# Performance work log

Hardware: AMD Instinct MI355X
Metric: run time of the kernel (lower is better)

## Reference

```python
import jax, jax.numpy as jnp
import numpy as np

B, L_SEQ = 2, 2048
D, H, DF, NL, V = 1024, 16, 4096, 3, 32000
E = D // H
EPS = 1e-5


def _ln(x, g, b):
    m = jnp.mean(x, axis=-1, keepdims=True)
    v = jnp.mean((x - m) ** 2, axis=-1, keepdims=True)
    return (x - m) * jax.lax.rsqrt(v + EPS) * g + b


def setup_inputs() -> dict:
    key = jax.random.key(0)
    ks = jax.random.split(key, 16)
    s = 0.02
    tokens = jax.random.randint(ks[0], (B, L_SEQ), 0, V)
    pad_mask = jnp.zeros((B, L_SEQ, 1), dtype=bool)
    inp = dict(
        tokens=tokens,
        pad_mask=pad_mask,
        tok_emb=jax.random.normal(ks[1], (V, D)) * s,
        pos_emb=jax.random.normal(ks[2], (L_SEQ, D)) * s,
        Wq=jax.random.normal(ks[3], (NL, D, D)) * s,
        bq=jnp.zeros((NL, D)),
        Wk=jax.random.normal(ks[4], (NL, D, D)) * s,
        bk=jnp.zeros((NL, D)),
        Wv=jax.random.normal(ks[5], (NL, D, D)) * s,
        bv=jnp.zeros((NL, D)),
        Wo=jax.random.normal(ks[6], (NL, D, D)) * s,
        bo=jnp.zeros((NL, D)),
        W1=jax.random.normal(ks[7], (NL, D, DF)) * s,
        b1=jnp.zeros((NL, DF)),
        W2=jax.random.normal(ks[8], (NL, DF, D)) * s,
        b2=jnp.zeros((NL, D)),
        ln1_g=jnp.ones((NL, D)), ln1_b=jnp.zeros((NL, D)),
        ln3_g=jnp.ones((NL, D)), ln3_b=jnp.zeros((NL, D)),
        lnf_g=jnp.ones((D,)), lnf_b=jnp.zeros((D,)),
        Wout=jax.random.normal(ks[9], (D, V)) * s,
        bout=jnp.zeros((V,)),
    )
    return inp


def reference(tokens, pad_mask, tok_emb, pos_emb, Wq, bq, Wk, bk, Wv, bv,
              Wo, bo, W1, b1, W2, b2, ln1_g, ln1_b, ln3_g, ln3_b,
              lnf_g, lnf_b, Wout, bout):
    Bb, Ls = tokens.shape
    x = tok_emb[tokens] + pos_emb[:Ls]  # [B,L,D]
    causal = jnp.triu(jnp.ones((Ls, Ls), dtype=bool), 1)
    # pad mask applied on keys, causal on (query,key); mask True = blocked
    mask = jnp.logical_or(pad_mask[:, :, 0][:, None, :], causal[None])  # [B,L,L]
    mask = mask[:, None]  # [B,1,L,L], broadcast over heads
    scale = 1.0 / np.sqrt(E)
    for i in range(NL):
        h = _ln(x, ln1_g[i], ln1_b[i])
        q = (h @ Wq[i] + bq[i]).reshape(Bb, Ls, H, E)
        k = (h @ Wk[i] + bk[i]).reshape(Bb, Ls, H, E)
        v = (h @ Wv[i] + bv[i]).reshape(Bb, Ls, H, E)
        scores = jnp.einsum('blhe,bshe->bhls', q, k)
        scores = jnp.where(mask, -jnp.inf, scores)
        A = jax.nn.softmax(scale * scores, axis=-1)
        A = jnp.where(mask, 0.0, A)
        o = jnp.einsum('bhls,bshd->blhd', A, v).reshape(Bb, Ls, D)
        x = x + (o @ Wo[i] + bo[i])
        h = _ln(x, ln3_g[i], ln3_b[i])
        h = jax.nn.gelu(h @ W1[i] + b1[i], approximate=False)
        x = x + (h @ W2[i] + b2[i])
    x = _ln(x, lnf_g, lnf_b)
    return x @ Wout + bout  # [B,L,V]
```

## Files before the change

kernel.cpp:

```cpp
#include <hip/hip_runtime.h>
#include <math.h>

#define D_    1024
#define H_    16
#define E_    64
#define DF_   4096
#define NL_   3
#define V_    32000
#define B_    2
#define LSEQ_ 2048
#define M_    (B_*LSEQ_)
#define QKVW  (3*D_)

#define OQKV  0
#define OWO   ((size_t)3072*1024)
#define OW1   ((size_t)4096*1024)
#define OW2   ((size_t)8192*1024)

typedef __attribute__((ext_vector_type(8))) short bf16x8;
typedef __attribute__((ext_vector_type(4))) float f32x4;
typedef __attribute__((ext_vector_type(4))) unsigned short us4_t;

__device__ __forceinline__ float bfr2f(unsigned short u){ return __uint_as_float(((unsigned)u)<<16); }
__device__ __forceinline__ unsigned short f2bfr(float f){
  unsigned u = __float_as_uint(f);
  u += 0x7fffu + ((u>>16)&1u);
  return (unsigned short)(u>>16);
}
__device__ __forceinline__ void gl_lds16(const unsigned short* g, unsigned short* l){
  __builtin_amdgcn_global_load_lds((const __attribute__((address_space(1))) void*)g,
                                   (__attribute__((address_space(3))) void*)l, 16, 0, 0);
}

__device__ __forceinline__ void row_ln_write(float4 v, const float* __restrict__ g,
                                             const float* __restrict__ b,
                                             unsigned short* __restrict__ hrow,
                                             float* red, int tid){
  const int wave = tid>>6, lane = tid&63;
  float s  = v.x+v.y+v.z+v.w;
  float s2 = v.x*v.x+v.y*v.y+v.z*v.z+v.w*v.w;
  #pragma unroll
  for (int off=1; off<64; off<<=1){ s += __shfl_xor(s,off); s2 += __shfl_xor(s2,off); }
  if (!lane){ red[wave]=s; red[4+wave]=s2; }
  __syncthreads();
  s  = red[0]+red[1]+red[2]+red[3];
  s2 = red[4]+red[5]+red[6]+red[7];
  const float mean = s*(1.f/D_);
  const float var  = s2*(1.f/D_) - mean*mean;
  const float rstd = rsqrtf(var + 1e-5f);
  float4 gg = ((const float4*)g)[tid];
  float4 bb = ((const float4*)b)[tid];
  us4_t ov;
  ov[0] = f2bfr((v.x-mean)*rstd*gg.x + bb.x);
  ov[1] = f2bfr((v.y-mean)*rstd*gg.y + bb.y);
  ov[2] = f2bfr((v.z-mean)*rstd*gg.z + bb.z);
  ov[3] = f2bfr((v.w-mean)*rstd*gg.w + bb.w);
  *(us4_t*)&hrow[tid*4] = ov;
}

__global__ __launch_bounds__(256) void embed_ln_kernel(const int* __restrict__ tokens,
                                                       const float* __restrict__ tok_emb,
                                                       const float* __restrict__ pos_emb,
                                                       const float* __restrict__ g,
                                                       const float* __restrict__ b,
                                                       float* __restrict__ x,
                                                       unsigned short* __restrict__ h){
  __shared__ float red[8];
  const int r = blockIdx.x, tid = threadIdx.x;
  const int l = r & (LSEQ_-1);
  const int t = tokens[r];
  float4 te = ((const float4*)(tok_emb + (size_t)t*D_))[tid];
  float4 pe = ((const float4*)(pos_emb + (size_t)l*D_))[tid];
  float4 o = {te.x+pe.x, te.y+pe.y, te.z+pe.z, te.w+pe.w};
  ((float4*)(x + (size_t)r*D_))[tid] = o;
  row_ln_write(o, g, b, h + (size_t)r*D_, red, tid);
}

__global__ __launch_bounds__(256) void ln_kernel(const float* __restrict__ x,
                                                 const float* __restrict__ g,
                                                 const float* __restrict__ b,
                                                 unsigned short* __restrict__ h){
  __shared__ float red[8];
  const int r = blockIdx.x, tid = threadIdx.x;
  float4 v = ((const float4*)(x + (size_t)r*D_))[tid];
  row_ln_write(v, g, b, h + (size_t)r*D_, red, tid);
}

__global__ __launch_bounds__(256) void reduce2_ln_kernel(float* __restrict__ x,
                                                         const float* __restrict__ pt,
                                                         const float* __restrict__ bias,
                                                         const float* __restrict__ g,
                                                         const float* __restrict__ b,
                                                         unsigned short* __restrict__ h){
  __shared__ float red[8];
  const int r = blockIdx.x, tid = threadIdx.x;
  const size_t i = ((size_t)r*D_ + tid*4);
  float4 xv = *(const float4*)(x + i);
  float4 p0 = *(const float4*)(pt + i);
  float4 p1 = *(const float4*)(pt + (size_t)M_*D_ + i);
  float4 bb = *(const float4*)(bias + tid*4);
  xv.x += p0.x + p1.x + bb.x;
  xv.y += p0.y + p1.y + bb.y;
  xv.z += p0.z + p1.z + bb.z;
  xv.w += p0.w + p1.w + bb.w;
  *(float4*)(x + i) = xv;
  row_ln_write(xv, g, b, h + (size_t)r*D_, red, tid);
}

__global__ __launch_bounds__(256) void transpose_layer_kernel(const float* __restrict__ Wq,
                                                              const float* __restrict__ Wk,
                                                              const float* __restrict__ Wv,
                                                              const float* __restrict__ Wo,
                                                              const float* __restrict__ W1,
                                                              const float* __restrict__ W2,
                                                              unsigned short* __restrict__ wt){
  __shared__ unsigned short T[64*65];
  const int bid = blockIdx.x, tid = threadIdx.x;
  const float* W; unsigned short* dst; int N, K, n0, k0;
  if (bid < 768){
    int z = bid>>8, t = bid&255;
    W = (z==0)?Wq:(z==1)?Wk:Wv; N=1024; K=1024;
    n0=(t&15)*64; k0=(t>>4)*64;
    dst = wt + OQKV + (size_t)z*1024*1024;
  } else if (bid < 1024){
    int t = bid-768; W=Wo; N=1024; K=1024;
    n0=(t&15)*64; k0=(t>>4)*64; dst = wt + OWO;
  } else if (bid < 2048){
    int t = bid-1024; W=W1; N=4096; K=1024;
    n0=(t&63)*64; k0=(t>>6)*64; dst = wt + OW1;
  } else {
    int t = bid-2048; W=W2; N=1024; K=4096;
    n0=(t&15)*64; k0=(t>>4)*64; dst = wt + OW2;
  }
  const int rr = tid>>4, c4 = (tid&15)*4;
  #pragma unroll
  for (int pp=0; pp<4; pp++){
    int row = pp*16 + rr;
    float4 f = *(const float4*)(W + (size_t)(k0+row)*N + n0 + c4);
    T[(c4+0)*65 + row] = f2bfr(f.x);
    T[(c4+1)*65 + row] = f2bfr(f.y);
    T[(c4+2)*65 + row] = f2bfr(f.z);
    T[(c4+3)*65 + row] = f2bfr(f.w);
  }
  __syncthreads();
  const int nr = tid>>2, kc = (tid&3)*16;
  bf16x8 o0, o1;
  #pragma unroll
  for (int j=0;j<8;j++){ o0[j] = (short)T[nr*65 + kc + j];
                         o1[j] = (short)T[nr*65 + kc + 8 + j]; }
  *(bf16x8*)&dst[(size_t)(n0+nr)*K + k0 + kc]     = o0;
  *(bf16x8*)&dst[(size_t)(n0+nr)*K + k0 + kc + 8] = o1;
}

__global__ __launch_bounds__(256) void transpose_kernel(const float* __restrict__ W,
                                                        unsigned short* __restrict__ WT,
                                                        int N, int K, int rowOff){
  __shared__ unsigned short T[64*65];
  const int n0 = blockIdx.x*64, k0 = blockIdx.y*64;
  const int tid = threadIdx.x;
  const int rr = tid>>4, c4 = (tid&15)*4;
  #pragma unroll
  for (int pp=0; pp<4; pp++){
    int row = pp*16 + rr;
    float4 f = *(const float4*)(W + (size_t)(k0+row)*N + n0 + c4);
    T[(c4+0)*65 + row] = f2bfr(f.x);
    T[(c4+1)*65 + row] = f2bfr(f.y);
    T[(c4+2)*65 + row] = f2bfr(f.z);
    T[(c4+3)*65 + row] = f2bfr(f.w);
  }
  __syncthreads();
  const int nr = tid>>2, kc = (tid&3)*16;
  bf16x8 o0, o1;
  #pragma unroll
  for (int j=0;j<8;j++){ o0[j] = (short)T[nr*65 + kc + j];
                         o1[j] = (short)T[nr*65 + kc + 8 + j]; }
  *(bf16x8*)&WT[(size_t)(rowOff+n0+nr)*K + k0 + kc]     = o0;
  *(bf16x8*)&WT[(size_t)(rowOff+n0+nr)*K + k0 + kc + 8] = o1;
}

__global__ void concat_bias3(const float* __restrict__ bq,
                             const float* __restrict__ bk,
                             const float* __restrict__ bv,
                             float* __restrict__ d){
  int i = blockIdx.x*256 + threadIdx.x;
  int layer = i / QKVW, j = i % QKVW;
  d[i] = (j < D_) ? bq[layer*D_+j] : (j < 2*D_) ? bk[layer*D_+j-D_] : bv[layer*D_+j-2*D_];
}

template<int EPI>
__global__ __launch_bounds__(256) void gemm_bt(const unsigned short* __restrict__ A,
                                               const unsigned short* __restrict__ Bt,
                                               const float* __restrict__ bias,
                                               unsigned short* __restrict__ Cb,
                                               float* __restrict__ Cf,
                                               int K, int Klen, int ldc){
  __shared__ unsigned short As[128*64];
  __shared__ unsigned short Bs[128*64];
  const int tid = threadIdx.x;
  const int wave = tid>>6, lane = tid&63;
  const int m0 = blockIdx.x*128, n0 = blockIdx.y*128;
  const int kbase = blockIdx.z * Klen;
  const int wr = wave>>1, wc = wave&1;
  const unsigned short* Ab = A + (size_t)m0*K + kbase;
  const unsigned short* Bb = Bt + (size_t)n0*K + kbase;
  f32x4 acc[4][4] = {};
  int srow[4], sk[4];
  #pragma unroll
  for (int i=0;i<4;i++){
    int ci = i*256 + tid;
    srow[i] = ci>>3;
    sk[i]   = ((ci&7) ^ (srow[i]&7))*8;
  }
  for (int kt=0; kt<Klen; kt+=64){
    __syncthreads();
    #pragma unroll
    for (int i=0;i<4;i++){
      gl_lds16(Ab + (size_t)srow[i]*K + kt + sk[i], As + i*2048 + wave*512);
      gl_lds16(Bb + (size_t)srow[i]*K + kt + sk[i], Bs + i*2048 + wave*512);
    }
    __syncthreads();
    #pragma unroll
    for (int ks=0; ks<2; ks++){
      bf16x8 af[4], bfv[4];
      #pragma unroll
      for (int mi=0;mi<4;mi++){
        int row = wr*64 + mi*16 + (lane&15);
        int ch  = (ks*4 + (lane>>4)) ^ (row&7);
        af[mi] = *(const bf16x8*)&As[row*64 + ch*8];
      }
      #pragma unroll
      for (int ni=0;ni<4;ni++){
        int row = wc*64 + ni*16 + (lane&15);
        int ch  = (ks*4 + (lane>>4)) ^ (row&7);
        bfv[ni] = *(const bf16x8*)&Bs[row*64 + ch*8];
      }
      #pragma unroll
      for (int mi=0;mi<4;mi++)
        #pragma unroll
        for (int ni=0;ni<4;ni++)
          acc[mi][ni] = __builtin_amdgcn_mfma_f32_16x16x32_bf16(af[mi], bfv[ni], acc[mi][ni], 0,0,0);
    }
  }
  const int rq = (lane>>4)*4, cq = lane&15;
  float* Cfz = (EPI==5) ? (Cf + (size_t)blockIdx.z*M_*D_) : Cf;
  #pragma unroll
  for (int mi=0;mi<4;mi++){
    #pragma unroll
    for (int j=0;j<4;j++){
      int r = m0 + wr*64 + mi*16 + rq + j;
      #pragma unroll
      for (int ni=0;ni<4;ni++){
        int c = n0 + wc*64 + ni*16 + cq;
        if (EPI==2)      Cf[(size_t)r*D_ + c] += acc[mi][ni][j] + bias[c];
        else if (EPI==5) Cfz[(size_t)r*ldc + c] = acc[mi][ni][j];
        else             Cf[(size_t)r*ldc + c] = acc[mi][ni][j] + bias[c];
      }
    }
  }
}

#define GBAR()  do{ __builtin_amdgcn_s_barrier(); __builtin_amdgcn_sched_barrier(0); }while(0)
#define GPHASE(P, STAGE_STMT, TAIL_STMT) do{                                        \
    bf16x8 afr[2][2];                                                               \
    _Pragma("unroll")                                                               \
    for (int mi=0;mi<2;mi++){                                                       \
      _Pragma("unroll")                                                             \
      for (int ks=0;ks<2;ks++){                                                     \
        int row = wr*128 + (P)*32 + mi*16 + (lane&15);                              \
        int ch  = (ks*4 + (lane>>4)) ^ (row&7);                                     \
        afr[mi][ks] = *(const bf16x8*)&Alds[row*64 + ch*8];                         \
      } }                                                                           \
    STAGE_STMT;                                                                     \
    GBAR();                                                                         \
    __builtin_amdgcn_s_setprio(1);                                                  \
    _Pragma("unroll")                                                               \
    for (int ks=0;ks<2;ks++){                                                       \
      _Pragma("unroll")                                                             \
      for (int mi=0;mi<2;mi++){                                                     \
        _Pragma("unroll")                                                           \
        for (int ni=0;ni<4;ni++)                                                    \
          acc[(P)*2+mi][ni] = __builtin_amdgcn_mfma_f32_16x16x32_bf16(              \
              afr[mi][ks], bfr[ni][ks], acc[(P)*2+mi][ni], 0,0,0);                  \
      } }                                                                           \
    __builtin_amdgcn_s_setprio(0);                                                  \
    __builtin_amdgcn_sched_barrier(0);                                              \
    TAIL_STMT;                                                                      \
  }while(0)

template<int EPI>
__global__ __launch_bounds__(512, 2) void gemm256(const unsigned short* __restrict__ A,
                                                  const unsigned short* __restrict__ Bt,
                                                  const float* __restrict__ bias,
                                                  unsigned short* __restrict__ Cb,
                                                  float* __restrict__ Cf,
                                                  int K, int ldc){
  __shared__ unsigned short lds[2][2][256*64];
  const int tid = threadIdx.x, wave = tid>>6, lane = tid&63;
  const int m0 = blockIdx.x*256, n0 = blockIdx.y*256;
  const int wr = wave>>2, wc = wave&3;
  const unsigned short* Ab = A  + (size_t)m0*K;
  const unsigned short* Bb = Bt + (size_t)n0*K;
  int srow[2], scol[2];
  #pragma unroll
  for (int i=0;i<2;i++){
    int ci = i*512 + tid;
    srow[i] = ci>>3;
    scol[i] = ((ci&7) ^ (srow[i]&7))*8;
  }
  auto stageA = [&](int tbuf, int hh, int kt){
    #pragma unroll
    for (int i=0;i<2;i++)
      gl_lds16(Ab + (size_t)(hh*128+srow[i])*K + kt + scol[i],
               &lds[tbuf][0][hh*8192 + (i*512+tid)*8]);
  };
  auto stageB = [&](int tbuf, int hh, int kt){
    #pragma unroll
    for (int i=0;i<2;i++)
      gl_lds16(Bb + (size_t)(hh*128+srow[i])*K + kt + scol[i],
               &lds[tbuf][1][hh*8192 + (i*512+tid)*8]);
  };
  f32x4 acc[8][4] = {};
  const int NT = K>>6;
  stageB(0,0,0); stageB(0,1,0);
  stageA(0,0,0); stageA(0,1,0);
  stageB(1,0,64); stageB(1,1,64);
  asm volatile("s_waitcnt vmcnt(4)" ::: "memory");
  __builtin_amdgcn_sched_barrier(0);
  GBAR();
  for (int t=0; t<NT; ++t){
    const int buf = t&1, bufn = buf^1;
    const unsigned short* Alds = &lds[buf][0][0];
    const unsigned short* Blds = &lds[buf][1][0];
    const int ktA = (t+1)<<6, ktB = (t+2)<<6;
    const bool s1 = (t+1)<NT, s2 = (t+2)<NT;
    bf16x8 bfr[4][2];
    #pragma unroll
    for (int ni=0;ni<4;ni++)
      #pragma unroll
      for (int ks=0;ks<2;ks++){
        int row = wc*64 + ni*16 + (lane&15);
        int ch  = (ks*4 + (lane>>4)) ^ (row&7);
        bfr[ni][ks] = *(const bf16x8*)&Blds[row*64 + ch*8];
      }
    GPHASE(0, if (s1) stageA(bufn,0,ktA), ((void)0));
    GPHASE(1, if (s1) stageA(bufn,1,ktA), ((void)0));
    GPHASE(2, if (s2) stageB(buf,0,ktB), ((void)0));
    GPHASE(3, if (s2) stageB(buf,1,ktB),
           { if (s2){ asm volatile("s_waitcnt vmcnt(4)" ::: "memory"); }
             else   { asm volatile("s_waitcnt vmcnt(0)" ::: "memory"); }
             __builtin_amdgcn_sched_barrier(0);
             GBAR(); });
  }
  const int rq = (lane>>4)*4, cq = lane&15;
  #pragma unroll
  for (int mi=0;mi<8;mi++){
    #pragma unroll
    for (int j=0;j<4;j++){
      int r = m0 + wr*128 + mi*16 + rq + j;
      #pragma unroll
      for (int ni=0;ni<4;ni++){
        int c = n0 + wc*64 + ni*16 + cq;
        float v = acc[mi][ni][j] + bias[c];
        if (EPI==0)      Cb[(size_t)r*ldc + c] = f2bfr(v);
        else if (EPI==1) Cb[(size_t)r*ldc + c] = f2bfr(0.5f*v*(1.f+erff(v*0.70710678f)));
        else             Cf[(size_t)r*ldc + c] = v;
      }
    }
  }
}

__global__ __launch_bounds__(512) void attn_kernel(const unsigned short* __restrict__ qkv,
                                                   unsigned short* __restrict__ o){
  int bid = blockIdx.x, qt, bh;
  if (bid < 256){ qt = bid & 15;        bh = bid >> 4; }
  else          { qt = 15 - (bid & 15); bh = 16 + ((bid - 256) >> 4); }
  const int b = bh>>4, h = bh&15;
  const int tid = threadIdx.x, wave = tid>>6, lane = tid&63;
  const int ql0 = qt*128;
  __shared__ unsigned short Qs[128*64];
  __shared__ unsigned short Ks[2][64*64];
  __shared__ unsigned short Vt[2][64*72];
  __shared__ unsigned short Ps[128*72];
  const size_t base = (size_t)b*LSEQ_*QKVW + (size_t)h*E_;
  const unsigned short* qb = qkv + base;
  const unsigned short* kb = qkv + base + D_;
  const unsigned short* vb = qkv + base + 2*D_;
  #pragma unroll
  for (int ii=0; ii<2; ii++){
    int i = wave + ii*8;
    int chunk = i*64 + lane, r = chunk>>3, cc = chunk&7;
    gl_lds16(qb + (size_t)(ql0 + r)*QKVW + ((cc^(r&7))*8), Qs + i*512);
  }
  const int kck = wave*64 + lane, kr = kck>>3, kc = kck&7;
  gl_lds16(kb + (size_t)kr*QKVW + ((kc^(kr&7))*8), &Ks[0][wave*512]);
  {
    bf16x8 vv = *(const bf16x8*)(vb + (size_t)lane*QKVW + wave*8);
    #pragma unroll
    for (int j=0;j<8;j++) Vt[0][(wave*8+j)*72 + lane] = (unsigned short)vv[j];
  }
  __syncthreads();
  float m4[4] = {-3e38f,-3e38f,-3e38f,-3e38f};
  float l4[4] = {0.f,0.f,0.f,0.f};
  f32x4 oacc[4] = {};
  const int nkv = qt*2 + 2;
  for (int t=0; t<nkv; t++){
    const int s0 = t*64, cur = t&1, nxt = cur^1;
    const bool more = (t+1) < nkv;
    bf16x8 vvn;
    if (more){
      const int s0n = s0 + 64;
      gl_lds16(kb + (size_t)(s0n + kr)*QKVW + ((kc^(kr&7))*8), &Ks[nxt][wave*512]);
      vvn = *(const bf16x8*)(vb + (size_t)(s0n + lane)*QKVW + wave*8);
    }
    __builtin_amdgcn_sched_barrier(0);
    f32x4 sacc[4] = {};
    __builtin_amdgcn_s_setprio(1);
    #pragma unroll
    for (int ks=0; ks<2; ks++){
      int qrow = wave*16 + (lane&15);
      int qc = ks*4 + (lane>>4);
      bf16x8 a = *(const bf16x8*)&Qs[qrow*64 + ((qc^(qrow&7))*8)];
      #pragma unroll
      for (int fc=0; fc<4; fc++){
        int krow = fc*16 + (lane&15);
        bf16x8 bv = *(const bf16x8*)&Ks[cur][krow*64 + ((qc^(krow&7))*8)];
        sacc[fc] = __builtin_amdgcn_mfma_f32_16x16x32_bf16(a, bv, sacc[fc], 0,0,0);
      }
    }
    __builtin_amdgcn_s_setprio(0);
    float rm[4];
    #pragma unroll
    for (int j=0;j<4;j++){
      int rowa = ql0 + wave*16 + (lane>>4)*4 + j;
      float mx = -3e38f;
      #pragma unroll
      for (int fc=0;fc<4;fc++){
        int cola = s0 + fc*16 + (lane&15);
        float sv = sacc[fc][j]*0.125f;
        if (cola > rowa) sv = -3e38f;
        sacc[fc][j] = sv;
        mx = fmaxf(mx, sv);
      }
      rm[j] = mx;
    }
    #pragma unroll
    for (int off=1; off<16; off<<=1)
      #pragma unroll
      for (int j=0;j<4;j++) rm[j] = fmaxf(rm[j], __shfl_xor(rm[j], off));
    bool need = (rm[0]>m4[0]+8.f)||(rm[1]>m4[1]+8.f)||(rm[2]>m4[2]+8.f)||(rm[3]>m4[3]+8.f);
    const bool rescale = (__ballot(need) != 0ull);
    float al[4] = {1.f,1.f,1.f,1.f};
    if (rescale){
      #pragma unroll
      for (int j=0;j<4;j++){
        float mn = fmaxf(m4[j], rm[j]);
        al[j] = __expf(m4[j] - mn);
        m4[j] = mn;
      }
    }
    float rs[4] = {0.f,0.f,0.f,0.f};
    #pragma unroll
    for (int fc=0;fc<4;fc++)
      #pragma unroll
      for (int j=0;j<4;j++){
        float pv = __expf(sacc[fc][j] - m4[j]);
        rs[j] += pv;
        Ps[(wave*16 + (lane>>4)*4 + j)*72 + fc*16 + (lane&15)] =
            (unsigned short)(__float_as_uint(pv)>>16);
      }
    #pragma unroll
    for (int off=1; off<16; off<<=1)
      #pragma unroll
      for (int j=0;j<4;j++) rs[j] += __shfl_xor(rs[j], off);
    if (rescale){
      #pragma unroll
      for (int j=0;j<4;j++){
        l4[j] = l4[j]*al[j] + rs[j];
        #pragma unroll
        for (int fc=0;fc<4;fc++) oacc[fc][j] *= al[j];
      }
    } else {
      #pragma unroll
      for (int j=0;j<4;j++) l4[j] += rs[j];
    }
    __builtin_amdgcn_s_setprio(1);
    #pragma unroll
    for (int ks=0; ks<2; ks++){
      bf16x8 ap = *(const bf16x8*)&Ps[(wave*16 + (lane&15))*72 + ks*32 + (lane>>4)*8];
      #pragma unroll
      for (int fc=0;fc<4;fc++){
        bf16x8 bv = *(const bf16x8*)&Vt[cur][(fc*16 + (lane&15))*72 + ks*32 + (lane>>4)*8];
        oacc[fc] = __builtin_amdgcn_mfma_f32_16x16x32_bf16(ap, bv, oacc[fc], 0,0,0);
      }
    }
    __builtin_amdgcn_s_setprio(0);
    if (more){
      #pragma unroll
      for (int j=0;j<8;j++) Vt[nxt][(wave*8+j)*72 + lane] = (unsigned short)vvn[j];
    }
    __syncthreads();
  }
  #pragma unroll
  for (int fc=0;fc<4;fc++)
    #pragma unroll
    for (int j=0;j<4;j++){
      int r = ql0 + wave*16 + (lane>>4)*4 + j;
      int c = h*E_ + fc*16 + (lane&15);
      o[((size_t)b*LSEQ_ + r)*D_ + c] = f2bfr(oacc[fc][j] / l4[j]);
    }
}

extern "C" void kernel_launch(void* const* d_in, const int* in_sizes, int n_in,
                              void* d_out, int out_size, void* d_ws, size_t ws_size,
                              hipStream_t stream){
  (void)in_sizes; (void)n_in; (void)out_size;
  const int*   tokens = (const int*)d_in[0];
  const float* tok_emb= (const float*)d_in[2];
  const float* pos_emb= (const float*)d_in[3];
  const float* Wq = (const float*)d_in[4];
  const float* bq = (const float*)d_in[5];
  const float* Wk = (const float*)d_in[6];
  const float* bk = (const float*)d_in[7];
  const float* Wv = (const float*)d_in[8];
  const float* bv = (const float*)d_in[9];
  const float* Wo = (const float*)d_in[10];
  const float* bo = (const float*)d_in[11];
  const float* W1 = (const float*)d_in[12];
  const float* b1 = (const float*)d_in[13];
  const float* W2 = (const float*)d_in[14];
  const float* b2 = (const float*)d_in[15];
  const float* ln1g = (const float*)d_in[16];
  const float* ln1b = (const float*)d_in[17];
  const float* ln3g = (const float*)d_in[18];
  const float* ln3b = (const float*)d_in[19];
  const float* lnfg = (const float*)d_in[20];
  const float* lnfb = (const float*)d_in[21];
  const float* Wout = (const float*)d_in[22];
  const float* bout = (const float*)d_in[23];

  char* p = (char*)d_ws;
  float* x             = (float*)p;           p += (size_t)M_*D_*sizeof(float);
  unsigned short* h    = (unsigned short*)p;  p += (size_t)M_*D_*2;
  unsigned short* qkv  = (unsigned short*)p;  p += (size_t)M_*QKVW*2;
  unsigned short* ob   = (unsigned short*)p;  p += (size_t)M_*D_*2;
  unsigned short* ffh  = (unsigned short*)p;  p += (size_t)M_*DF_*2;
  unsigned short* wt   = (unsigned short*)p;  p += (size_t)V_*D_*2;
  float* bqkv3         = (float*)p;           p += (size_t)NL_*QKVW*sizeof(float);
  if ((size_t)(p - (char*)d_ws) > ws_size) return;
  float* pt = (float*)qkv;

  embed_ln_kernel<<<M_, 256, 0, stream>>>(tokens, tok_emb, pos_emb, ln1g, ln1b, x, h);
  concat_bias3<<<NL_*QKVW/256, 256, 0, stream>>>(bq, bk, bv, bqkv3);
  for (int i=0;i<NL_;i++){
    const size_t wOff  = (size_t)i*D_*D_;
    const size_t w1Off = (size_t)i*D_*DF_;
    transpose_layer_kernel<<<3072, 256, 0, stream>>>(Wq + wOff, Wk + wOff, Wv + wOff,
                                                     Wo + wOff, W1 + w1Off, W2 + w1Off, wt);
    gemm256<0><<<dim3(M_/256, QKVW/256), 512, 0, stream>>>(h, wt + OQKV, bqkv3 + i*QKVW, qkv, nullptr, D_, QKVW);
    attn_kernel<<<512, 512, 0, stream>>>(qkv, ob);
    gemm_bt<2><<<dim3(M_/128, D_/128), 256, 0, stream>>>(ob, wt + OWO, bo + i*D_, nullptr, x, D_, D_, D_);
    ln_kernel<<<M_, 256, 0, stream>>>(x, ln3g + i*D_, ln3b + i*D_, h);
    gemm256<1><<<dim3(M_/256, DF_/256), 512, 0, stream>>>(h, wt + OW1, b1 + i*DF_, ffh, nullptr, D_, DF_);
    gemm_bt<5><<<dim3(M_/128, D_/128, 2), 256, 0, stream>>>(ffh, wt + OW2, nullptr, nullptr, pt, DF_, DF_/2, D_);
    reduce2_ln_kernel<<<M_, 256, 0, stream>>>(x, pt, b2 + i*D_,
                                              (i < NL_-1) ? ln1g + (i+1)*D_ : lnfg,
                                              (i < NL_-1) ? ln1b + (i+1)*D_ : lnfb, h);
  }
  transpose_kernel<<<dim3(V_/64, D_/64), 256, 0, stream>>>(Wout, wt, V_, D_, 0);
  gemm256<3><<<dim3(M_/256, V_/256), 512, 0, stream>>>(h, wt, bout, nullptr, (float*)d_out, D_, V_);
}
```

Before: 1.152 ms.

## Compute softmax row sums via an extra ones-column MFMA and skip masking off-diagonal tiles

The attention kernel appends 16 rows of bf16 ones to the transposed V tile so a fifth MFMA column block accumulates the softmax denominator. This removes the per-tile row-sum reductions and shuffles. Causal masking is now applied only to tiles that touch the diagonal. The GEMM phase also gains an explicit lgkmcnt wait before its MFMAs. In exchange, the denominator now sums bf16-rounded probabilities, which costs some precision, and each tile does one extra MFMA per k-step plus extra LDS.

Result: faster. 1.099 ms (-4.6%).

```diff
diff --git a/kernel.cpp b/kernel.cpp
--- a/kernel.cpp
+++ b/kernel.cpp
@@ -272,6 +272,8 @@
       } }                                                                           \
     STAGE_STMT;                                                                     \
     GBAR();                                                                         \
+    asm volatile("s_waitcnt lgkmcnt(0)" ::: "memory");                              \
+    __builtin_amdgcn_sched_barrier(0);                                              \
     __builtin_amdgcn_s_setprio(1);                                                  \
     _Pragma("unroll")                                                               \
     for (int ks=0;ks<2;ks++){                                                       \
@@ -379,7 +381,7 @@
   const int ql0 = qt*128;
   __shared__ unsigned short Qs[128*64];
   __shared__ unsigned short Ks[2][64*64];
-  __shared__ unsigned short Vt[2][64*72];
+  __shared__ unsigned short Vt[2][80*72];
   __shared__ unsigned short Ps[128*72];
   const size_t base = (size_t)b*LSEQ_*QKVW + (size_t)h*E_;
   const unsigned short* qb = qkv + base;
@@ -391,6 +393,11 @@
     int chunk = i*64 + lane, r = chunk>>3, cc = chunk&7;
     gl_lds16(qb + (size_t)(ql0 + r)*QKVW + ((cc^(r&7))*8), Qs + i*512);
   }
+  for (int i = tid; i < 2*16*72; i += 512){
+    int bufi = (i >= 16*72);
+    int rem  = i - bufi*16*72;
+    Vt[bufi][(64 + rem/72)*72 + (rem%72)] = 0x3F80;
+  }
   const int kck = wave*64 + lane, kr = kck>>3, kc = kck&7;
   gl_lds16(kb + (size_t)kr*QKVW + ((kc^(kr&7))*8), &Ks[0][wave*512]);
   {
@@ -400,8 +407,7 @@
   }
   __syncthreads();
   float m4[4] = {-3e38f,-3e38f,-3e38f,-3e38f};
-  float l4[4] = {0.f,0.f,0.f,0.f};
-  f32x4 oacc[4] = {};
+  f32x4 oacc[5] = {};
   const int nkv = qt*2 + 2;
   for (int t=0; t<nkv; t++){
     const int s0 = t*64, cur = t&1, nxt = cur^1;
@@ -429,19 +435,33 @@
     }
     __builtin_amdgcn_s_setprio(0);
     float rm[4];
-    #pragma unroll
-    for (int j=0;j<4;j++){
-      int rowa = ql0 + wave*16 + (lane>>4)*4 + j;
-      float mx = -3e38f;
-      #pragma unroll
-      for (int fc=0;fc<4;fc++){
-        int cola = s0 + fc*16 + (lane&15);
-        float sv = sacc[fc][j]*0.125f;
-        if (cola > rowa) sv = -3e38f;
-        sacc[fc][j] = sv;
-        mx = fmaxf(mx, sv);
-      }
-      rm[j] = mx;
+    if (s0 + 63 > ql0 + wave*16){
+      #pragma unroll
+      for (int j=0;j<4;j++){
+        int rowa = ql0 + wave*16 + (lane>>4)*4 + j;
+        float mx = -3e38f;
+        #pragma unroll
+        for (int fc=0;fc<4;fc++){
+          int cola = s0 + fc*16 + (lane&15);
+          float sv = sacc[fc][j]*0.125f;
+          if (cola > rowa) sv = -3e38f;
+          sacc[fc][j] = sv;
+          mx = fmaxf(mx, sv);
+        }
+        rm[j] = mx;
+      }
+    } else {
+      #pragma unroll
+      for (int j=0;j<4;j++){
+        float mx = -3e38f;
+        #pragma unroll
+        for (int fc=0;fc<4;fc++){
+          float sv = sacc[fc][j]*0.125f;
+          sacc[fc][j] = sv;
+          mx = fmaxf(mx, sv);
+        }
+        rm[j] = mx;
+      }
     }
     #pragma unroll
     for (int off=1; off<16; off<<=1)
@@ -449,46 +469,33 @@
       for (int j=0;j<4;j++) rm[j] = fmaxf(rm[j], __shfl_xor(rm[j], off));
     bool need = (rm[0]>m4[0]+8.f)||(rm[1]>m4[1]+8.f)||(rm[2]>m4[2]+8.f)||(rm[3]>m4[3]+8.f);
     const bool rescale = (__ballot(need) != 0ull);
-    float al[4] = {1.f,1.f,1.f,1.f};
     if (rescale){
+      float al[4];
       #pragma unroll
       for (int j=0;j<4;j++){
         float mn = fmaxf(m4[j], rm[j]);
         al[j] = __expf(m4[j] - mn);
         m4[j] = mn;
       }
-    }
-    float rs[4] = {0.f,0.f,0.f,0.f};
+      #pragma unroll
+      for (int fc=0;fc<5;fc++)
+        #pragma unroll
+        for (int j=0;j<4;j++) oacc[fc][j] *= al[j];
+    }
     #pragma unroll
     for (int fc=0;fc<4;fc++)
       #pragma unroll
       for (int j=0;j<4;j++){
         float pv = __expf(sacc[fc][j] - m4[j]);
-        rs[j] += pv;
         Ps[(wave*16 + (lane>>4)*4 + j)*72 + fc*16 + (lane&15)] =
             (unsigned short)(__float_as_uint(pv)>>16);
       }
-    #pragma unroll
-    for (int off=1; off<16; off<<=1)
-      #pragma unroll
-      for (int j=0;j<4;j++) rs[j] += __shfl_xor(rs[j], off);
-    if (rescale){
-      #pragma unroll
-      for (int j=0;j<4;j++){
-        l4[j] = l4[j]*al[j] + rs[j];
-        #pragma unroll
-        for (int fc=0;fc<4;fc++) oacc[fc][j] *= al[j];
-      }
-    } else {
-      #pragma unroll
-      for (int j=0;j<4;j++) l4[j] += rs[j];
-    }
     __builtin_amdgcn_s_setprio(1);
     #pragma unroll
     for (int ks=0; ks<2; ks++){
       bf16x8 ap = *(const bf16x8*)&Ps[(wave*16 + (lane&15))*72 + ks*32 + (lane>>4)*8];
       #pragma unroll
-      for (int fc=0;fc<4;fc++){
+      for (int fc=0;fc<5;fc++){
         bf16x8 bv = *(const bf16x8*)&Vt[cur][(fc*16 + (lane&15))*72 + ks*32 + (lane>>4)*8];
         oacc[fc] = __builtin_amdgcn_mfma_f32_16x16x32_bf16(ap, bv, oacc[fc], 0,0,0);
       }
@@ -506,7 +513,7 @@
     for (int j=0;j<4;j++){
       int r = ql0 + wave*16 + (lane>>4)*4 + j;
       int c = h*E_ + fc*16 + (lane&15);
-      o[((size_t)b*LSEQ_ + r)*D_ + c] = f2bfr(oacc[fc][j] / l4[j]);
+      o[((size_t)b*LSEQ_ + r)*D_ + c] = f2bfr(oacc[fc][j] / oacc[4][j]);
     }
 }
 
```
